# Kernel tuning notes

Hardware: AMD Instinct MI355X
Metric: run time of the kernel (lower is better)

Reference implementation:

```python
import jax, jax.numpy as jnp
import numpy as np

N_QUBITS = 4
N_LAYERS = 2


def setup_inputs() -> dict:
    key = jax.random.key(0)
    ks = jax.random.split(key, 8)
    B, S, D, H, O = 64, 4096, 20, 64, 3
    rn = lambda k, shape: jax.random.normal(k, shape, dtype=jnp.float32)
    sc = lambda fan: np.float32(1.0 / np.sqrt(fan))
    return {
        "x": rn(ks[0], (B, S, D)),
        "W_embed": rn(ks[1], (H, D)) * sc(D),
        "b_embed": jnp.zeros((H,), jnp.float32),
        "W_c2q": rn(ks[2], (N_QUBITS, H)) * sc(H),
        "b_c2q": jnp.zeros((N_QUBITS,), jnp.float32),
        "q_weights": rn(ks[3], (N_LAYERS, N_QUBITS, 3)) * np.float32(0.1),
        "W_q2c": rn(ks[4], (H, N_QUBITS)) * sc(N_QUBITS),
        "b_q2c": jnp.zeros((H,), jnp.float32),
        "W_out": rn(ks[5], (O, H)) * sc(H),
        "b_out": jnp.zeros((O,), jnp.float32),
    }


def _rot_matrix(phi, theta, omega):
    # PennyLane Rot(phi, theta, omega) = RZ(omega) @ RY(theta) @ RZ(phi)
    c = jnp.cos(theta * 0.5)
    s = jnp.sin(theta * 0.5)
    ep = jnp.exp(-0.5j * (phi + omega))  # e^{-i(phi+omega)/2}
    em = jnp.exp(-0.5j * (phi - omega))  # e^{-i(phi-omega)/2}
    row0 = jnp.stack([ep * c, -jnp.conj(em) * s])
    row1 = jnp.stack([em * s, jnp.conj(ep) * c])
    return jnp.stack([row0, row1]).astype(jnp.complex64)  # [2,2]


def _apply_1q(state, U, q):
    # state: [N,2,2,2,2], U: [2,2] shared across the batch
    ax = 1 + q
    s = jnp.moveaxis(state, ax, -1)
    s = jnp.einsum('...a,ba->...b', s, U)
    return jnp.moveaxis(s, -1, ax)


def _cnot(state, q):
    # control qubit q (axis 1+q), target qubit q+1 (axis 2+q)
    ac = 1 + q
    s0 = jnp.take(state, 0, axis=ac)
    # after removing control axis, the target axis index becomes ac
    s1 = jnp.flip(jnp.take(state, 1, axis=ac), axis=ac)
    return jnp.stack([s0, s1], axis=ac)


def _quantum_layer(q_in, weights):
    # q_in: [N, n_qubits] angles; weights: [n_layers, n_qubits, 3]
    half = q_in * 0.5
    v = jnp.stack([jnp.cos(half), jnp.sin(half)], axis=-1).astype(jnp.complex64)  # [N,4,2]
    # RY(inputs[i]) applied to |0...0> -> product state
    state = jnp.einsum('na,nb,nc,nd->nabcd', v[:, 0], v[:, 1], v[:, 2], v[:, 3])
    for layer in range(N_LAYERS):
        for q in range(N_QUBITS):
            U = _rot_matrix(weights[layer, q, 0], weights[layer, q, 1], weights[layer, q, 2])
            state = _apply_1q(state, U, q)
        for q in range(N_QUBITS - 1):
            state = _cnot(state, q)
    probs = state.real ** 2 + state.imag ** 2  # [N,2,2,2,2]
    z = []
    for q in range(N_QUBITS):
        axes = tuple(a for a in range(1, N_QUBITS + 1) if a != 1 + q)
        p = jnp.sum(probs, axis=axes)  # [N,2]
        z.append(p[:, 0] - p[:, 1])   # <Z_q>
    return jnp.stack(z, axis=-1)  # [N, n_qubits]


def reference(x, W_embed, b_embed, W_c2q, b_c2q, q_weights, W_q2c, b_q2c, W_out, b_out):
    B, S, _ = x.shape
    h = jax.nn.relu(jnp.einsum('bsd,hd->bsh', x, W_embed) + b_embed)      # [B,S,H]
    q_in = jnp.tanh(jnp.einsum('bsh,qh->bsq', h, W_c2q) + b_c2q)          # [B,S,4]
    z = _quantum_layer(q_in.reshape(B * S, N_QUBITS), q_weights)          # [B*S,4]
    z = z.reshape(B, S, N_QUBITS)
    h2 = jnp.einsum('bsq,hq->bsh', z, W_q2c) + b_q2c                      # [B,S,H]
    coords = jnp.einsum('bsh,oh->bso', h2, W_out) + b_out                 # [B,S,3]
    return coords
```

## Files before the change

### kernel.cpp

```cpp
#include <hip/hip_runtime.h>

typedef __bf16 bf16x8 __attribute__((ext_vector_type(8)));
typedef float f32x4 __attribute__((ext_vector_type(4)));
typedef float f32x2 __attribute__((ext_vector_type(2)));

__device__ __attribute__((aligned(16))) float g_C01[162];
__device__ float g_C2[81];
__device__ float g_off[3];

#define NQ 4
#define NLAYERS 2

__global__ __launch_bounds__(256) void precompute_kernel(
    const float* __restrict__ qw,
    const float* __restrict__ Wq2c,
    const float* __restrict__ bq2c,
    const float* __restrict__ Wout,
    const float* __restrict__ bout) {
  __shared__ float Ucoef[8][8];
  __shared__ float Ur[16][16];
  __shared__ float Ui[16][16];
  __shared__ float A[4][16][16];
  __shared__ float Wc[3][4];
  const int tid = threadIdx.x;

  if (tid < 64) {
    const int gate = tid >> 3, comp = tid & 7;
    const float phi   = qw[gate * 3 + 0];
    const float theta = qw[gate * 3 + 1];
    const float omega = qw[gate * 3 + 2];
    const float cs = (comp == 2 || comp == 3 || comp == 4 || comp == 5)
                         ? __sinf(0.5f * theta)
                         : __cosf(0.5f * theta);
    const float ang = (comp == 2 || comp == 3 || comp == 4 || comp == 5)
                          ? -0.5f * (phi - omega)
                          : -0.5f * (phi + omega);
    const float tr = ((comp & 1) == 0) ? __cosf(ang) : __sinf(ang);
    const float sgn = (comp == 2 || comp == 7) ? -1.f : 1.f;
    Ucoef[gate][comp] = sgn * tr * cs;
  }
  __syncthreads();

  const int col = tid >> 4, amp = tid & 15;
  float re = (amp == col) ? 1.f : 0.f, im = 0.f;
#pragma unroll
  for (int layer = 0; layer < NLAYERS; ++layer) {
#pragma unroll
    for (int q = 0; q < NQ; ++q) {
      const int gate = layer * NQ + q;
      const int bit = 8 >> q;
      const bool lo = !(amp & bit);
      const float cr1 = lo ? Ucoef[gate][0] : Ucoef[gate][6];
      const float ci1 = lo ? Ucoef[gate][1] : Ucoef[gate][7];
      const float cr2 = lo ? Ucoef[gate][2] : Ucoef[gate][4];
      const float ci2 = lo ? Ucoef[gate][3] : Ucoef[gate][5];
      const float pr = __shfl_xor(re, bit);
      const float pi = __shfl_xor(im, bit);
      const float mr = re, mi = im;
      re = cr1 * mr - ci1 * mi + cr2 * pr - ci2 * pi;
      im = cr1 * mi + ci1 * mr + cr2 * pi + ci2 * pr;
    }
#pragma unroll
    for (int q = 0; q < NQ - 1; ++q) {
      const int cb = 8 >> q, tb = 4 >> q;
      const float pr = __shfl_xor(re, tb);
      const float pi = __shfl_xor(im, tb);
      if (amp & cb) { re = pr; im = pi; }
    }
  }
  Ur[amp][col] = re;
  Ui[amp][col] = im;
  __syncthreads();

  for (int e = tid; e < 4 * 16 * 16; e += blockDim.x) {
    const int q = e >> 8, i = (e >> 4) & 15, j = e & 15;
    float s = 0.f;
    for (int k = 0; k < 16; ++k) {
      const float d = ((k >> (3 - q)) & 1) ? -1.f : 1.f;
      s += d * (Ur[k][i] * Ur[k][j] + Ui[k][i] * Ui[k][j]);
    }
    A[q][i][j] = s;
  }
  if (tid < 12) {
    const int o = tid >> 2, q = tid & 3;
    float s = 0.f;
    for (int h = 0; h < 64; ++h) s += Wout[o * 64 + h] * Wq2c[h * 4 + q];
    Wc[o][q] = s;
  }
  if (tid < 3) {
    float s = bout[tid];
    for (int h = 0; h < 64; ++h) s += Wout[tid * 64 + h] * bq2c[h];
    g_off[tid] = s;
  }
  __syncthreads();

  for (int e = tid; e < 243; e += blockDim.x) {
    const int o = e / 81, t = e % 81;
    const int tv0 = t / 27, tv1 = (t / 9) % 3, tv2 = (t / 3) % 3, tv3 = t % 3;
    const int tv[4] = {tv0, tv1, tv2, tv3};
    int xmask = 0, zmask = 0;
    for (int q = 0; q < 4; ++q) {
      const int b = 8 >> q;
      if (tv[q] == 2) xmask |= b;
      else if (tv[q] == 1) zmask |= b;
    }
    float s = 0.f;
    for (int i = 0; i < 16; ++i) {
      const int j = i ^ xmask;
      const float sgn = (__popc(i & zmask) & 1) ? -1.f : 1.f;
      const float g = Wc[o][0] * A[0][i][j] + Wc[o][1] * A[1][i][j] +
                      Wc[o][2] * A[2][i][j] + Wc[o][3] * A[3][i][j];
      s += sgn * g;
    }
    const float val = s * 0.0625f;
    if (o == 0) g_C01[2 * t] = val;
    else if (o == 1) g_C01[2 * t + 1] = val;
    else g_C2[t] = val;
  }
}

__device__ __forceinline__ float fast_tanh(float v) {
  const float e = __expf(2.f * v);
  return 1.f - 2.f * __builtin_amdgcn_rcpf(e + 1.f);
}

__global__ __launch_bounds__(256, 4) void fused_kernel(
    const float* __restrict__ x,
    const float* __restrict__ Wemb,
    const float* __restrict__ bemb,
    const float* __restrict__ Wc2q,
    const float* __restrict__ bc2q,
    float* __restrict__ out, int N) {
  __shared__ float xs[4][1280];

  const int tid = blockIdx.x * 256 + threadIdx.x;
  const int lane = threadIdx.x & 63;
  const int warp = threadIdx.x >> 6;
  const int wbase = (tid >> 6) << 6;
  if (wbase >= N) return;
  const int g = lane >> 4;
  const int cc = lane & 15;

  const f32x4 zero4 = {0.f, 0.f, 0.f, 0.f};

  {
    const float4* x4 = reinterpret_cast<const float4*>(x);
    float4* ls4 = reinterpret_cast<float4*>(&xs[warp][0]);
    const size_t base4 = (size_t)wbase * 5;
    const size_t max4 = (size_t)N * 5 - 1;
#pragma unroll
    for (int i = 0; i < 5; ++i) {
      size_t gi = base4 + (size_t)(i * 64 + lane);
      ls4[i * 64 + lane] = x4[gi <= max4 ? gi : max4];
    }
  }

  bf16x8 Aemb[4];
#pragma unroll
  for (int ht = 0; ht < 4; ++ht) {
    const int h = ht * 16 + cc;
    const float* wr = Wemb + h * 20;
    float t0 = 0.f, t1 = 0.f, t2 = 0.f, t3 = 0.f, t4 = 0.f, t5 = 0.f, t6 = 0.f, t7 = 0.f;
    if (g < 2) {
      const float4 v0 = *(const float4*)(wr + g * 8);
      const float4 v1 = *(const float4*)(wr + g * 8 + 4);
      t0 = v0.x; t1 = v0.y; t2 = v0.z; t3 = v0.w;
      t4 = v1.x; t5 = v1.y; t6 = v1.z; t7 = v1.w;
    } else if (g == 2) {
      const float4 v0 = *(const float4*)(wr + 16);
      t0 = v0.x; t1 = v0.y; t2 = v0.z; t3 = v0.w;
      t4 = bemb[h];
    }
    Aemb[ht][0] = (__bf16)t0; Aemb[ht][1] = (__bf16)t1;
    Aemb[ht][2] = (__bf16)t2; Aemb[ht][3] = (__bf16)t3;
    Aemb[ht][4] = (__bf16)t4; Aemb[ht][5] = (__bf16)t5;
    Aemb[ht][6] = (__bf16)t6; Aemb[ht][7] = (__bf16)t7;
  }

  bf16x8 A2[2];
#pragma unroll
  for (int t = 0; t < 2; ++t) {
#pragma unroll
    for (int j = 0; j < 8; ++j) {
      const int mu = t * 32 + ((j >> 2) << 4) + (g << 2) + (j & 3);
      A2[t][j] = (__bf16)Wc2q[(cc & 3) * 64 + mu];
    }
  }

  f32x4 av = zero4;
#pragma unroll
  for (int rt = 0; rt < 4; ++rt) {
    const int el = rt * 16 + cc;
    const float* ep = &xs[warp][el * 20];
    float t0 = 0.f, t1 = 0.f, t2 = 0.f, t3 = 0.f, t4 = 0.f, t5 = 0.f, t6 = 0.f, t7 = 0.f;
    if (g < 2) {
      const float4 v0 = *(const float4*)(ep + g * 8);
      const float4 v1 = *(const float4*)(ep + g * 8 + 4);
      t0 = v0.x; t1 = v0.y; t2 = v0.z; t3 = v0.w;
      t4 = v1.x; t5 = v1.y; t6 = v1.z; t7 = v1.w;
    } else if (g == 2) {
      const float4 v0 = *(const float4*)(ep + 16);
      t0 = v0.x; t1 = v0.y; t2 = v0.z; t3 = v0.w;
      t4 = 1.f;
    }
    bf16x8 B;
    B[0] = (__bf16)t0; B[1] = (__bf16)t1; B[2] = (__bf16)t2; B[3] = (__bf16)t3;
    B[4] = (__bf16)t4; B[5] = (__bf16)t5; B[6] = (__bf16)t6; B[7] = (__bf16)t7;

    const f32x4 acc0 = __builtin_amdgcn_mfma_f32_16x16x32_bf16(Aemb[0], B, zero4, 0, 0, 0);
    const f32x4 acc1 = __builtin_amdgcn_mfma_f32_16x16x32_bf16(Aemb[1], B, zero4, 0, 0, 0);
    const f32x4 acc2 = __builtin_amdgcn_mfma_f32_16x16x32_bf16(Aemb[2], B, zero4, 0, 0, 0);
    const f32x4 acc3 = __builtin_amdgcn_mfma_f32_16x16x32_bf16(Aemb[3], B, zero4, 0, 0, 0);

    bf16x8 P0, P1;
#pragma unroll
    for (int j = 0; j < 8; ++j) {
      P0[j] = (__bf16)fmaxf(((j >> 2) ? acc1 : acc0)[j & 3], 0.f);
      P1[j] = (__bf16)fmaxf(((j >> 2) ? acc3 : acc2)[j & 3], 0.f);
    }
    f32x4 a2 = __builtin_amdgcn_mfma_f32_16x16x32_bf16(A2[0], P0, zero4, 0, 0, 0);
    a2 = __builtin_amdgcn_mfma_f32_16x16x32_bf16(A2[1], P1, a2, 0, 0, 0);

    if (g == rt) av = a2;
  }

  const float a0 = fast_tanh(av[0] + bc2q[0]);
  const float a1 = fast_tanh(av[1] + bc2q[1]);
  const float a2v = fast_tanh(av[2] + bc2q[2]);
  const float a3 = fast_tanh(av[3] + bc2q[3]);

  const float f0v[3] = {1.f, __cosf(a0), __sinf(a0)};
  const float f1v[3] = {1.f, __cosf(a1), __sinf(a1)};
  const float f2v[3] = {1.f, __cosf(a2v), __sinf(a2v)};
  const float f3v[3] = {1.f, __cosf(a3), __sinf(a3)};

  float T23[9];
#pragma unroll
  for (int i2 = 0; i2 < 3; ++i2)
#pragma unroll
    for (int i3 = 0; i3 < 3; ++i3) T23[i2 * 3 + i3] = f2v[i2] * f3v[i3];
  float T[27];
#pragma unroll
  for (int i1 = 0; i1 < 3; ++i1)
#pragma unroll
    for (int k = 0; k < 9; ++k) T[i1 * 9 + k] = f1v[i1] * T23[k];

  f32x2 y01 = {g_off[0], g_off[1]};
  float y2 = g_off[2];
#pragma unroll
  for (int i0 = 0; i0 < 3; ++i0) {
    f32x2 s01 = {0.f, 0.f};
    float s2 = 0.f;
#pragma unroll
    for (int k = 0; k < 27; ++k) {
      const float tv = T[k];
      const f32x2 c01 = *reinterpret_cast<const f32x2*>(&g_C01[2 * (i0 * 27 + k)]);
      s01 += c01 * tv;
      s2 = fmaf(g_C2[i0 * 27 + k], tv, s2);
    }
    y01 += s01 * f0v[i0];
    y2 = fmaf(f0v[i0], s2, y2);
  }

  const int eo = wbase + lane;
  if (eo < N) {
    out[eo * 3 + 0] = y01[0];
    out[eo * 3 + 1] = y01[1];
    out[eo * 3 + 2] = y2;
  }
}

extern "C" void kernel_launch(void* const* d_in, const int* in_sizes, int n_in,
                              void* d_out, int out_size, void* d_ws, size_t ws_size,
                              hipStream_t stream) {
  const float* x    = (const float*)d_in[0];
  const float* Wemb = (const float*)d_in[1];
  const float* bemb = (const float*)d_in[2];
  const float* Wc2q = (const float*)d_in[3];
  const float* bc2q = (const float*)d_in[4];
  const float* qw   = (const float*)d_in[5];
  const float* Wq2c = (const float*)d_in[6];
  const float* bq2c = (const float*)d_in[7];
  const float* Wout = (const float*)d_in[8];
  const float* bout = (const float*)d_in[9];
  float* out = (float*)d_out;

  const int N = in_sizes[0] / 20;

  hipLaunchKernelGGL(precompute_kernel, dim3(1), dim3(256), 0, stream,
                     qw, Wq2c, bq2c, Wout, bout);
  hipLaunchKernelGGL(fused_kernel, dim3((N + 255) / 256), dim3(256), 0, stream,
                     x, Wemb, bemb, Wc2q, bc2q, out, N);
}
```

Measured before the change: 20.74 us.

## Fuse precompute into main kernel, stage x via registers with swizzled LDS, vectorize stores

Removes the separate single-block precompute launch and has every block recompute the quantum-circuit coefficient tables in shared memory, overlapping with its x loads. The sign-weighted A matrices are collapsed into three G matrices using per-output weights, reducing work per block. The x tile is loaded into registers first and written to LDS with an XOR swizzle and padding so the bias/zero lanes need no branches. Coefficients are read as float4 from LDS and outputs are staged through LDS for coalesced float4 stores. Redundant per-block precompute and extra syncthreads add cost in exchange for removing a kernel launch and serialization.

Result: slower. 25.42 us (+22.5%).

```diff
diff --git a/kernel.cpp b/kernel.cpp
--- a/kernel.cpp
+++ b/kernel.cpp
@@ -4,120 +4,15 @@
 typedef float f32x4 __attribute__((ext_vector_type(4)));
 typedef float f32x2 __attribute__((ext_vector_type(2)));
 
-__device__ __attribute__((aligned(16))) float g_C01[162];
-__device__ float g_C2[81];
-__device__ float g_off[3];
-
 #define NQ 4
 #define NLAYERS 2
 
-__global__ __launch_bounds__(256) void precompute_kernel(
-    const float* __restrict__ qw,
-    const float* __restrict__ Wq2c,
-    const float* __restrict__ bq2c,
-    const float* __restrict__ Wout,
-    const float* __restrict__ bout) {
-  __shared__ float Ucoef[8][8];
-  __shared__ float Ur[16][16];
-  __shared__ float Ui[16][16];
-  __shared__ float A[4][16][16];
-  __shared__ float Wc[3][4];
-  const int tid = threadIdx.x;
-
-  if (tid < 64) {
-    const int gate = tid >> 3, comp = tid & 7;
-    const float phi   = qw[gate * 3 + 0];
-    const float theta = qw[gate * 3 + 1];
-    const float omega = qw[gate * 3 + 2];
-    const float cs = (comp == 2 || comp == 3 || comp == 4 || comp == 5)
-                         ? __sinf(0.5f * theta)
-                         : __cosf(0.5f * theta);
-    const float ang = (comp == 2 || comp == 3 || comp == 4 || comp == 5)
-                          ? -0.5f * (phi - omega)
-                          : -0.5f * (phi + omega);
-    const float tr = ((comp & 1) == 0) ? __cosf(ang) : __sinf(ang);
-    const float sgn = (comp == 2 || comp == 7) ? -1.f : 1.f;
-    Ucoef[gate][comp] = sgn * tr * cs;
-  }
-  __syncthreads();
-
-  const int col = tid >> 4, amp = tid & 15;
-  float re = (amp == col) ? 1.f : 0.f, im = 0.f;
-#pragma unroll
-  for (int layer = 0; layer < NLAYERS; ++layer) {
-#pragma unroll
-    for (int q = 0; q < NQ; ++q) {
-      const int gate = layer * NQ + q;
-      const int bit = 8 >> q;
-      const bool lo = !(amp & bit);
-      const float cr1 = lo ? Ucoef[gate][0] : Ucoef[gate][6];
-      const float ci1 = lo ? Ucoef[gate][1] : Ucoef[gate][7];
-      const float cr2 = lo ? Ucoef[gate][2] : Ucoef[gate][4];
-      const float ci2 = lo ? Ucoef[gate][3] : Ucoef[gate][5];
-      const float pr = __shfl_xor(re, bit);
-      const float pi = __shfl_xor(im, bit);
-      const float mr = re, mi = im;
-      re = cr1 * mr - ci1 * mi + cr2 * pr - ci2 * pi;
-      im = cr1 * mi + ci1 * mr + cr2 * pi + ci2 * pr;
-    }
-#pragma unroll
-    for (int q = 0; q < NQ - 1; ++q) {
-      const int cb = 8 >> q, tb = 4 >> q;
-      const float pr = __shfl_xor(re, tb);
-      const float pi = __shfl_xor(im, tb);
-      if (amp & cb) { re = pr; im = pi; }
-    }
-  }
-  Ur[amp][col] = re;
-  Ui[amp][col] = im;
-  __syncthreads();
-
-  for (int e = tid; e < 4 * 16 * 16; e += blockDim.x) {
-    const int q = e >> 8, i = (e >> 4) & 15, j = e & 15;
-    float s = 0.f;
-    for (int k = 0; k < 16; ++k) {
-      const float d = ((k >> (3 - q)) & 1) ? -1.f : 1.f;
-      s += d * (Ur[k][i] * Ur[k][j] + Ui[k][i] * Ui[k][j]);
-    }
-    A[q][i][j] = s;
-  }
-  if (tid < 12) {
-    const int o = tid >> 2, q = tid & 3;
-    float s = 0.f;
-    for (int h = 0; h < 64; ++h) s += Wout[o * 64 + h] * Wq2c[h * 4 + q];
-    Wc[o][q] = s;
-  }
-  if (tid < 3) {
-    float s = bout[tid];
-    for (int h = 0; h < 64; ++h) s += Wout[tid * 64 + h] * bq2c[h];
-    g_off[tid] = s;
-  }
-  __syncthreads();
-
-  for (int e = tid; e < 243; e += blockDim.x) {
-    const int o = e / 81, t = e % 81;
-    const int tv0 = t / 27, tv1 = (t / 9) % 3, tv2 = (t / 3) % 3, tv3 = t % 3;
-    const int tv[4] = {tv0, tv1, tv2, tv3};
-    int xmask = 0, zmask = 0;
-    for (int q = 0; q < 4; ++q) {
-      const int b = 8 >> q;
-      if (tv[q] == 2) xmask |= b;
-      else if (tv[q] == 1) zmask |= b;
-    }
-    float s = 0.f;
-    for (int i = 0; i < 16; ++i) {
-      const int j = i ^ xmask;
-      const float sgn = (__popc(i & zmask) & 1) ? -1.f : 1.f;
-      const float g = Wc[o][0] * A[0][i][j] + Wc[o][1] * A[1][i][j] +
-                      Wc[o][2] * A[2][i][j] + Wc[o][3] * A[3][i][j];
-      s += sgn * g;
-    }
-    const float val = s * 0.0625f;
-    if (o == 0) g_C01[2 * t] = val;
-    else if (o == 1) g_C01[2 * t + 1] = val;
-    else g_C2[t] = val;
-  }
-}
+#define OFF_UCOEF 0
+#define OFF_WC    64
+#define OFF_UR    96
+#define OFF_UI    352
+#define OFF_W     608
+#define OFF_G     704
 
 __device__ __forceinline__ float fast_tanh(float v) {
   const float e = __expf(2.f * v);
@@ -130,28 +25,37 @@
     const float* __restrict__ bemb,
     const float* __restrict__ Wc2q,
     const float* __restrict__ bc2q,
+    const float* __restrict__ qw,
+    const float* __restrict__ Wq2c,
+    const float* __restrict__ bq2c,
+    const float* __restrict__ Wout,
+    const float* __restrict__ bout,
     float* __restrict__ out, int N) {
-  __shared__ float xs[4][1280];
-
-  const int tid = blockIdx.x * 256 + threadIdx.x;
-  const int lane = threadIdx.x & 63;
-  const int warp = threadIdx.x >> 6;
-  const int wbase = (tid >> 6) << 6;
-  if (wbase >= N) return;
+  __shared__ __attribute__((aligned(16))) float smem[4 * 2048];
+  __shared__ __attribute__((aligned(16))) float Cs01[3 * 56];
+  __shared__ __attribute__((aligned(16))) float Cs2[3 * 28];
+  __shared__ float offsS[3];
+
+  if ((int)(blockIdx.x << 8) >= N) return;
+
+  const int tid = threadIdx.x;
+  const int lane = tid & 63;
+  const int warp = tid >> 6;
+  const int wbase = (int)(blockIdx.x << 8) + (warp << 6);
   const int g = lane >> 4;
   const int cc = lane & 15;
-
+  float* ws = &smem[warp * 2048];
   const f32x4 zero4 = {0.f, 0.f, 0.f, 0.f};
 
+  float4 xr[5];
   {
     const float4* x4 = reinterpret_cast<const float4*>(x);
-    float4* ls4 = reinterpret_cast<float4*>(&xs[warp][0]);
+    const size_t max4 = (size_t)N * 5 - 1;
     const size_t base4 = (size_t)wbase * 5;
-    const size_t max4 = (size_t)N * 5 - 1;
 #pragma unroll
     for (int i = 0; i < 5; ++i) {
       size_t gi = base4 + (size_t)(i * 64 + lane);
-      ls4[i * 64 + lane] = x4[gi <= max4 ? gi : max4];
+      xr[i] = x4[gi <= max4 ? gi : max4];
     }
   }
 
@@ -187,25 +91,143 @@
     }
   }
 
+  if (tid < 64) {
+    const int gate = tid >> 3, comp = tid & 7;
+    const float phi   = qw[gate * 3 + 0];
+    const float theta = qw[gate * 3 + 1];
+    const float omega = qw[gate * 3 + 2];
+    const bool mid = (comp >= 2 && comp <= 5);
+    const float cs = mid ? __sinf(0.5f * theta) : __cosf(0.5f * theta);
+    const float ang = mid ? -0.5f * (phi - omega) : -0.5f * (phi + omega);
+    const float tr = ((comp & 1) == 0) ? __cosf(ang) : __sinf(ang);
+    const float sgn = (comp == 2 || comp == 7) ? -1.f : 1.f;
+    smem[OFF_UCOEF + gate * 8 + comp] = sgn * tr * cs;
+  } else if (tid < 76) {
+    const int e = tid - 64, o = e >> 2, q = e & 3;
+    float s = 0.f;
+    for (int h = 0; h < 64; ++h) s += Wout[o * 64 + h] * Wq2c[h * 4 + q];
+    smem[OFF_WC + e] = s;
+  } else if (tid < 79) {
+    const int o = tid - 76;
+    float s = bout[o];
+    for (int h = 0; h < 64; ++h) s += Wout[o * 64 + h] * bq2c[h];
+    offsS[o] = s;
+  }
+  __syncthreads();
+
+  {
+    const int col = tid >> 4, amp = tid & 15;
+    float re = (amp == col) ? 1.f : 0.f, im = 0.f;
+#pragma unroll
+    for (int layer = 0; layer < NLAYERS; ++layer) {
+#pragma unroll
+      for (int q = 0; q < NQ; ++q) {
+        const int gate = layer * NQ + q;
+        const int bit = 8 >> q;
+        const bool lo = !(amp & bit);
+        const float cr1 = smem[OFF_UCOEF + gate * 8 + (lo ? 0 : 6)];
+        const float ci1 = smem[OFF_UCOEF + gate * 8 + (lo ? 1 : 7)];
+        const float cr2 = smem[OFF_UCOEF + gate * 8 + (lo ? 2 : 4)];
+        const float ci2 = smem[OFF_UCOEF + gate * 8 + (lo ? 3 : 5)];
+        const float pr = __shfl_xor(re, bit);
+        const float pi = __shfl_xor(im, bit);
+        const float mr = re, mi = im;
+        re = cr1 * mr - ci1 * mi + cr2 * pr - ci2 * pi;
+        im = cr1 * mi + ci1 * mr + cr2 * pi + ci2 * pr;
+      }
+#pragma unroll
+      for (int q = 0; q < NQ - 1; ++q) {
+        const int cb = 8 >> q, tb = 4 >> q;
+        const float pr = __shfl_xor(re, tb);
+        const float pi = __shfl_xor(im, tb);
+        if (amp & cb) { re = pr; im = pi; }
+      }
+    }
+    smem[OFF_UR + amp * 16 + col] = re;
+    smem[OFF_UI + amp * 16 + col] = im;
+  }
+  if (tid < 48) {
+    const int o = tid >> 4, k = tid & 15;
+    float s = 0.f;
+#pragma unroll
+    for (int q = 0; q < NQ; ++q) {
+      const float t = smem[OFF_WC + o * 4 + q];
+      s += ((k >> (3 - q)) & 1) ? -t : t;
+    }
+    smem[OFF_W + tid] = s;
+  }
+  __syncthreads();
+
+  {
+    const int i = tid >> 4, j = tid & 15;
+    float s0 = 0.f, s1 = 0.f, s2 = 0.f;
+#pragma unroll
+    for (int k = 0; k < 16; ++k) {
+      const float S = smem[OFF_UR + k * 16 + i] * smem[OFF_UR + k * 16 + j] +
+                      smem[OFF_UI + k * 16 + i] * smem[OFF_UI + k * 16 + j];
+      s0 = fmaf(smem[OFF_W + k], S, s0);
+      s1 = fmaf(smem[OFF_W + 16 + k], S, s1);
+      s2 = fmaf(smem[OFF_W + 32 + k], S, s2);
+    }
+    smem[OFF_G + (i * 16 + j)] = s0;
+    smem[OFF_G + 256 + (i * 16 + j)] = s1;
+    smem[OFF_G + 512 + (i * 16 + j)] = s2;
+  }
+  __syncthreads();
+
+  if (tid < 243) {
+    const int o = tid / 81, t = tid % 81;
+    const int tv0 = t / 27, tv1 = (t / 9) % 3, tv2 = (t / 3) % 3, tv3 = t % 3;
+    const int tv[4] = {tv0, tv1, tv2, tv3};
+    int xmask = 0, zmask = 0;
+#pragma unroll
+    for (int q = 0; q < 4; ++q) {
+      const int b = 8 >> q;
+      if (tv[q] == 2) xmask |= b;
+      else if (tv[q] == 1) zmask |= b;
+    }
+    float s = 0.f;
+#pragma unroll
+    for (int i = 0; i < 16; ++i) {
+      const float sgn = (__popc(i & zmask) & 1) ? -1.f : 1.f;
+      s += sgn * smem[OFF_G + o * 256 + i * 16 + (i ^ xmask)];
+    }
+    const float val = s * 0.0625f;
+    if (o < 2) Cs01[tv0 * 56 + 2 * (t % 27) + o] = val;
+    else Cs2[tv0 * 28 + (t % 27)] = val;
+  } else if (tid < 249) {
+    const int p = tid - 243;
+    Cs01[(p >> 1) * 56 + 54 + (p & 1)] = 0.f;
+  } else if (tid < 252) {
+    Cs2[(tid - 249) * 28 + 27] = 0.f;
+  }
+  __syncthreads();
+
+  {
+#pragma unroll
+    for (int i = 0; i < 5; ++i) {
+      const int m = i * 64 + lane;
+      const int el = m / 5, ch = m % 5;
+      *(float4*)&ws[el * 32 + ((ch * 4) ^ ((el & 7) << 2))] = xr[i];
+    }
+    const float4 bias4 = {1.f, 0.f, 0.f, 0.f};
+    const float4 z4 = {0.f, 0.f, 0.f, 0.f};
+    const int sw = (lane & 7) << 2;
+    *(float4*)&ws[lane * 32 + ((5 * 4) ^ sw)] = bias4;
+    *(float4*)&ws[lane * 32 + ((6 * 4) ^ sw)] = z4;
+    *(float4*)&ws[lane * 32 + ((7 * 4) ^ sw)] = z4;
+  }
+
   f32x4 av = zero4;
 #pragma unroll
   for (int rt = 0; rt < 4; ++rt) {
     const int el = rt * 16 + cc;
-    const float* ep = &xs[warp][el * 20];
-    float t0 = 0.f, t1 = 0.f, t2 = 0.f, t3 = 0.f, t4 = 0.f, t5 = 0.f, t6 = 0.f, t7 = 0.f;
-    if (g < 2) {
-      const float4 v0 = *(const float4*)(ep + g * 8);
-      const float4 v1 = *(const float4*)(ep + g * 8 + 4);
-      t0 = v0.x; t1 = v0.y; t2 = v0.z; t3 = v0.w;
-      t4 = v1.x; t5 = v1.y; t6 = v1.z; t7 = v1.w;
-    } else if (g == 2) {
-      const float4 v0 = *(const float4*)(ep + 16);
-      t0 = v0.x; t1 = v0.y; t2 = v0.z; t3 = v0.w;
-      t4 = 1.f;
-    }
+    const int sw = (el & 7) << 2;
+    const float4 u0 = *(const float4*)&ws[el * 32 + ((g * 8 + 0) ^ sw)];
+    const float4 u1 = *(const float4*)&ws[el * 32 + ((g * 8 + 4) ^ sw)];
     bf16x8 B;
-    B[0] = (__bf16)t0; B[1] = (__bf16)t1; B[2] = (__bf16)t2; B[3] = (__bf16)t3;
-    B[4] = (__bf16)t4; B[5] = (__bf16)t5; B[6] = (__bf16)t6; B[7] = (__bf16)t7;
+    B[0] = (__bf16)u0.x; B[1] = (__bf16)u0.y; B[2] = (__bf16)u0.z; B[3] = (__bf16)u0.w;
+    B[4] = (__bf16)u1.x; B[5] = (__bf16)u1.y; B[6] = (__bf16)u1.z; B[7] = (__bf16)u1.w;
 
     const f32x4 acc0 = __builtin_amdgcn_mfma_f32_16x16x32_bf16(Aemb[0], B, zero4, 0, 0, 0);
     const f32x4 acc1 = __builtin_amdgcn_mfma_f32_16x16x32_bf16(Aemb[1], B, zero4, 0, 0, 0);
@@ -239,34 +261,54 @@
   for (int i2 = 0; i2 < 3; ++i2)
 #pragma unroll
     for (int i3 = 0; i3 < 3; ++i3) T23[i2 * 3 + i3] = f2v[i2] * f3v[i3];
-  float T[27];
+  float T[28];
 #pragma unroll
   for (int i1 = 0; i1 < 3; ++i1)
 #pragma unroll
     for (int k = 0; k < 9; ++k) T[i1 * 9 + k] = f1v[i1] * T23[k];
-
-  f32x2 y01 = {g_off[0], g_off[1]};
-  float y2 = g_off[2];
+  T[27] = 0.f;
+
+  f32x2 y01 = {offsS[0], offsS[1]};
+  float y2 = offsS[2];
 #pragma unroll
   for (int i0 = 0; i0 < 3; ++i0) {
     f32x2 s01 = {0.f, 0.f};
-    float s2 = 0.f;
-#pragma unroll
-    for (int k = 0; k < 27; ++k) {
-      const float tv = T[k];
-      const f32x2 c01 = *reinterpret_cast<const f32x2*>(&g_C01[2 * (i0 * 27 + k)]);
-      s01 += c01 * tv;
-      s2 = fmaf(g_C2[i0 * 27 + k], tv, s2);
+#pragma unroll
+    for (int kk = 0; kk < 14; ++kk) {
+      const float4 cp = *(const float4*)&Cs01[i0 * 56 + kk * 4];
+      const f32x2 lo = {cp.x, cp.y};
+      const f32x2 hi = {cp.z, cp.w};
+      s01 += lo * T[2 * kk];
+      s01 += hi * T[2 * kk + 1];
+    }
+    float s2v = 0.f;
+#pragma unroll
+    for (int kk = 0; kk < 7; ++kk) {
+      const float4 c2 = *(const float4*)&Cs2[i0 * 28 + kk * 4];
+      s2v = fmaf(c2.x, T[4 * kk + 0], s2v);
+      s2v = fmaf(c2.y, T[4 * kk + 1], s2v);
+      s2v = fmaf(c2.z, T[4 * kk + 2], s2v);
+      s2v = fmaf(c2.w, T[4 * kk + 3], s2v);
     }
     y01 += s01 * f0v[i0];
-    y2 = fmaf(f0v[i0], s2, y2);
-  }
-
-  const int eo = wbase + lane;
-  if (eo < N) {
-    out[eo * 3 + 0] = y01[0];
-    out[eo * 3 + 1] = y01[1];
-    out[eo * 3 + 2] = y2;
+    y2 = fmaf(f0v[i0], s2v, y2);
+  }
+
+  if (wbase + 64 <= N) {
+    ws[lane * 3 + 0] = y01[0];
+    ws[lane * 3 + 1] = y01[1];
+    ws[lane * 3 + 2] = y2;
+    if (lane < 48) {
+      const float4 v = *(const float4*)&ws[lane * 4];
+      reinterpret_cast<float4*>(out + (size_t)wbase * 3)[lane] = v;
+    }
+  } else {
+    const int eo = wbase + lane;
+    if (eo < N) {
+      out[eo * 3 + 0] = y01[0];
+      out[eo * 3 + 1] = y01[1];
+      out[eo * 3 + 2] = y2;
+    }
   }
 }
 
@@ -287,8 +329,6 @@
 
   const int N = in_sizes[0] / 20;
 
-  hipLaunchKernelGGL(precompute_kernel, dim3(1), dim3(256), 0, stream,
-                     qw, Wq2c, bq2c, Wout, bout);
   hipLaunchKernelGGL(fused_kernel, dim3((N + 255) / 256), dim3(256), 0, stream,
-                     x, Wemb, bemb, Wc2q, bc2q, out, N);
+                     x, Wemb, bemb, Wc2q, bc2q, qw, Wq2c, bq2c, Wout, bout, out, N);
 }
```

## Load x directly into LDS, fold biases into MFMA accumulators, coalesce output stores

Applied to the files above, without the earlier changes.

Full warps now move x tiles with global_load_lds straight into shared memory, skipping the register round trip. The embedding and c2q biases go into the MFMA accumulator inputs instead of an extra K element and scalar adds. Outputs are staged in LDS and written as coalesced float4 stores. The risks are the explicit vmcnt wait, which stalls until all loads finish, and extra bias loads inside the loop.

Measured after the change: 25.70 us. +23.9%, slower.

```diff
diff --git a/kernel.cpp b/kernel.cpp
--- a/kernel.cpp
+++ b/kernel.cpp
@@ -131,7 +131,7 @@
     const float* __restrict__ Wc2q,
     const float* __restrict__ bc2q,
     float* __restrict__ out, int N) {
-  __shared__ float xs[4][1280];
+  __shared__ __attribute__((aligned(16))) float smem[4][1280];
 
   const int tid = blockIdx.x * 256 + threadIdx.x;
   const int lane = threadIdx.x & 63;
@@ -140,18 +140,27 @@
   if (wbase >= N) return;
   const int g = lane >> 4;
   const int cc = lane & 15;
+  float* ws = &smem[warp][0];
+  const bool full = (wbase + 64 <= N);
 
   const f32x4 zero4 = {0.f, 0.f, 0.f, 0.f};
 
-  {
-    const float4* x4 = reinterpret_cast<const float4*>(x);
-    float4* ls4 = reinterpret_cast<float4*>(&xs[warp][0]);
-    const size_t base4 = (size_t)wbase * 5;
-    const size_t max4 = (size_t)N * 5 - 1;
+  if (full) {
+    const float4* x4 = reinterpret_cast<const float4*>(x) + (size_t)wbase * 5;
 #pragma unroll
     for (int i = 0; i < 5; ++i) {
-      size_t gi = base4 + (size_t)(i * 64 + lane);
-      ls4[i * 64 + lane] = x4[gi <= max4 ? gi : max4];
+      __builtin_amdgcn_global_load_lds(
+          (const __attribute__((address_space(1))) void*)(x4 + i * 64 + lane),
+          (__attribute__((address_space(3))) void*)(ws + i * 256), 16, 0, 0);
+    }
+  } else {
+#pragma unroll
+    for (int i = 0; i < 5; ++i) {
+      const int m = i * 64 + lane;
+      const int eg = wbase + m / 5;
+      float4 v = make_float4(0.f, 0.f, 0.f, 0.f);
+      if (eg < N) v = reinterpret_cast<const float4*>(x)[(size_t)eg * 5 + m % 5];
+      *(float4*)&ws[m * 4] = v;
     }
   }
 
@@ -169,7 +178,6 @@
     } else if (g == 2) {
       const float4 v0 = *(const float4*)(wr + 16);
       t0 = v0.x; t1 = v0.y; t2 = v0.z; t3 = v0.w;
-      t4 = bemb[h];
     }
     Aemb[ht][0] = (__bf16)t0; Aemb[ht][1] = (__bf16)t1;
     Aemb[ht][2] = (__bf16)t2; Aemb[ht][3] = (__bf16)t3;
@@ -187,47 +195,53 @@
     }
   }
 
+  const float4 bq = *(const float4*)bc2q;
+  f32x4 Cq;
+  Cq[0] = bq.x; Cq[1] = bq.y; Cq[2] = bq.z; Cq[3] = bq.w;
+
+  asm volatile("s_waitcnt vmcnt(0)" ::: "memory");
+
   f32x4 av = zero4;
 #pragma unroll
   for (int rt = 0; rt < 4; ++rt) {
     const int el = rt * 16 + cc;
-    const float* ep = &xs[warp][el * 20];
-    float t0 = 0.f, t1 = 0.f, t2 = 0.f, t3 = 0.f, t4 = 0.f, t5 = 0.f, t6 = 0.f, t7 = 0.f;
+    bf16x8 B;
+#pragma unroll
+    for (int j = 0; j < 8; ++j) B[j] = (__bf16)0.f;
     if (g < 2) {
-      const float4 v0 = *(const float4*)(ep + g * 8);
-      const float4 v1 = *(const float4*)(ep + g * 8 + 4);
-      t0 = v0.x; t1 = v0.y; t2 = v0.z; t3 = v0.w;
-      t4 = v1.x; t5 = v1.y; t6 = v1.z; t7 = v1.w;
+      const float4 u0 = *(const float4*)&ws[el * 20 + g * 8];
+      const float4 u1 = *(const float4*)&ws[el * 20 + g * 8 + 4];
+      B[0] = (__bf16)u0.x; B[1] = (__bf16)u0.y; B[2] = (__bf16)u0.z; B[3] = (__bf16)u0.w;
+      B[4] = (__bf16)u1.x; B[5] = (__bf16)u1.y; B[6] = (__bf16)u1.z; B[7] = (__bf16)u1.w;
     } else if (g == 2) {
-      const float4 v0 = *(const float4*)(ep + 16);
-      t0 = v0.x; t1 = v0.y; t2 = v0.z; t3 = v0.w;
-      t4 = 1.f;
-    }
-    bf16x8 B;
-    B[0] = (__bf16)t0; B[1] = (__bf16)t1; B[2] = (__bf16)t2; B[3] = (__bf16)t3;
-    B[4] = (__bf16)t4; B[5] = (__bf16)t5; B[6] = (__bf16)t6; B[7] = (__bf16)t7;
-
-    const f32x4 acc0 = __builtin_amdgcn_mfma_f32_16x16x32_bf16(Aemb[0], B, zero4, 0, 0, 0);
-    const f32x4 acc1 = __builtin_amdgcn_mfma_f32_16x16x32_bf16(Aemb[1], B, zero4, 0, 0, 0);
-    const f32x4 acc2 = __builtin_amdgcn_mfma_f32_16x16x32_bf16(Aemb[2], B, zero4, 0, 0, 0);
-    const f32x4 acc3 = __builtin_amdgcn_mfma_f32_16x16x32_bf16(Aemb[3], B, zero4, 0, 0, 0);
+      const float4 u0 = *(const float4*)&ws[el * 20 + 16];
+      B[0] = (__bf16)u0.x; B[1] = (__bf16)u0.y; B[2] = (__bf16)u0.z; B[3] = (__bf16)u0.w;
+    }
+
+    f32x4 acc[4];
+#pragma unroll
+    for (int ht = 0; ht < 4; ++ht) {
+      const float4 bi = *(const float4*)(bemb + ht * 16 + g * 4);
+      f32x4 ci; ci[0] = bi.x; ci[1] = bi.y; ci[2] = bi.z; ci[3] = bi.w;
+      acc[ht] = __builtin_amdgcn_mfma_f32_16x16x32_bf16(Aemb[ht], B, ci, 0, 0, 0);
+    }
 
     bf16x8 P0, P1;
 #pragma unroll
     for (int j = 0; j < 8; ++j) {
-      P0[j] = (__bf16)fmaxf(((j >> 2) ? acc1 : acc0)[j & 3], 0.f);
-      P1[j] = (__bf16)fmaxf(((j >> 2) ? acc3 : acc2)[j & 3], 0.f);
-    }
-    f32x4 a2 = __builtin_amdgcn_mfma_f32_16x16x32_bf16(A2[0], P0, zero4, 0, 0, 0);
+      P0[j] = (__bf16)fmaxf(((j >> 2) ? acc[1] : acc[0])[j & 3], 0.f);
+      P1[j] = (__bf16)fmaxf(((j >> 2) ? acc[3] : acc[2])[j & 3], 0.f);
+    }
+    f32x4 a2 = __builtin_amdgcn_mfma_f32_16x16x32_bf16(A2[0], P0, Cq, 0, 0, 0);
     a2 = __builtin_amdgcn_mfma_f32_16x16x32_bf16(A2[1], P1, a2, 0, 0, 0);
 
     if (g == rt) av = a2;
   }
 
-  const float a0 = fast_tanh(av[0] + bc2q[0]);
-  const float a1 = fast_tanh(av[1] + bc2q[1]);
-  const float a2v = fast_tanh(av[2] + bc2q[2]);
-  const float a3 = fast_tanh(av[3] + bc2q[3]);
+  const float a0 = fast_tanh(av[0]);
+  const float a1 = fast_tanh(av[1]);
+  const float a2v = fast_tanh(av[2]);
+  const float a3 = fast_tanh(av[3]);
 
   const float f0v[3] = {1.f, __cosf(a0), __sinf(a0)};
   const float f1v[3] = {1.f, __cosf(a1), __sinf(a1)};
@@ -262,11 +276,21 @@
     y2 = fmaf(f0v[i0], s2, y2);
   }
 
-  const int eo = wbase + lane;
-  if (eo < N) {
-    out[eo * 3 + 0] = y01[0];
-    out[eo * 3 + 1] = y01[1];
-    out[eo * 3 + 2] = y2;
+  if (full) {
+    ws[lane * 3 + 0] = y01[0];
+    ws[lane * 3 + 1] = y01[1];
+    ws[lane * 3 + 2] = y2;
+    if (lane < 48) {
+      const float4 v = *(const float4*)&ws[lane * 4];
+      reinterpret_cast<float4*>(out + (size_t)wbase * 3)[lane] = v;
+    }
+  } else {
+    const int eo = wbase + lane;
+    if (eo < N) {
+      out[eo * 3 + 0] = y01[0];
+      out[eo * 3 + 1] = y01[1];
+      out[eo * 3 + 2] = y2;
+    }
   }
 }
 
```

## Process two 64-row groups per warp with prefetched x and swizzled LDS layout

Applied to the files above, without the earlier changes.

Each warp now handles two groups of 64 rows. The second group's x tile is loaded into registers while the first group's MFMA pipeline runs, so global load latency is hidden and the per-warp weight-fragment setup is amortized over twice as many rows. The LDS staging layout changes to a 32-float padded, XOR-swizzled row with the bias/zero padding written explicitly, which removes the g-dependent branches when building B fragments. The grid is halved, and the extra registers and larger shared tile may reduce occupancy.

After: 26.83 us. 29.3% more time.

```diff
diff --git a/kernel.cpp b/kernel.cpp
--- a/kernel.cpp
+++ b/kernel.cpp
@@ -124,6 +124,116 @@
   return 1.f - 2.f * __builtin_amdgcn_rcpf(e + 1.f);
 }
 
+
+__device__ __forceinline__ void load_x_group(const float* __restrict__ x,
+                                             int wbase, int lane, int N,
+                                             float4 xr[5]) {
+  const float4* x4 = reinterpret_cast<const float4*>(x);
+  const size_t max4 = (size_t)N * 5 - 1;
+  const size_t base4 = (size_t)wbase * 5;
+#pragma unroll
+  for (int i = 0; i < 5; ++i) {
+    size_t gi = base4 + (size_t)(i * 64 + lane);
+    xr[i] = x4[gi <= max4 ? gi : max4];
+  }
+}
+
+__device__ __forceinline__ void stage_x(float* ws, int lane, const float4 xr[5]) {
+#pragma unroll
+  for (int i = 0; i < 5; ++i) {
+    const int m = i * 64 + lane;
+    const int el = m / 5, ch = m % 5;
+    *(float4*)&ws[el * 32 + ((ch * 4) ^ ((el & 7) << 2))] = xr[i];
+  }
+  const float4 bias4 = {1.f, 0.f, 0.f, 0.f};
+  const float4 z4 = {0.f, 0.f, 0.f, 0.f};
+  const int sw = (lane & 7) << 2;
+  *(float4*)&ws[lane * 32 + ((5 * 4) ^ sw)] = bias4;
+  *(float4*)&ws[lane * 32 + ((6 * 4) ^ sw)] = z4;
+  *(float4*)&ws[lane * 32 + ((7 * 4) ^ sw)] = z4;
+}
+
+__device__ __forceinline__ f32x4 compute_group(const float* ws, int g, int cc,
+                                               const bf16x8 Aemb[4],
+                                               const bf16x8 A2[2]) {
+  const f32x4 zero4 = {0.f, 0.f, 0.f, 0.f};
+  f32x4 av = zero4;
+#pragma unroll
+  for (int rt = 0; rt < 4; ++rt) {
+    const int el = rt * 16 + cc;
+    const int sw = (el & 7) << 2;
+    const float4 u0 = *(const float4*)&ws[el * 32 + ((g * 8 + 0) ^ sw)];
+    const float4 u1 = *(const float4*)&ws[el * 32 + ((g * 8 + 4) ^ sw)];
+    bf16x8 B;
+    B[0] = (__bf16)u0.x; B[1] = (__bf16)u0.y; B[2] = (__bf16)u0.z; B[3] = (__bf16)u0.w;
+    B[4] = (__bf16)u1.x; B[5] = (__bf16)u1.y; B[6] = (__bf16)u1.z; B[7] = (__bf16)u1.w;
+
+    const f32x4 acc0 = __builtin_amdgcn_mfma_f32_16x16x32_bf16(Aemb[0], B, zero4, 0, 0, 0);
+    const f32x4 acc1 = __builtin_amdgcn_mfma_f32_16x16x32_bf16(Aemb[1], B, zero4, 0, 0, 0);
+    const f32x4 acc2 = __builtin_amdgcn_mfma_f32_16x16x32_bf16(Aemb[2], B, zero4, 0, 0, 0);
+    const f32x4 acc3 = __builtin_amdgcn_mfma_f32_16x16x32_bf16(Aemb[3], B, zero4, 0, 0, 0);
+
+    bf16x8 P0, P1;
+#pragma unroll
+    for (int j = 0; j < 8; ++j) {
+      P0[j] = (__bf16)fmaxf(((j >> 2) ? acc1 : acc0)[j & 3], 0.f);
+      P1[j] = (__bf16)fmaxf(((j >> 2) ? acc3 : acc2)[j & 3], 0.f);
+    }
+    f32x4 a2 = __builtin_amdgcn_mfma_f32_16x16x32_bf16(A2[0], P0, zero4, 0, 0, 0);
+    a2 = __builtin_amdgcn_mfma_f32_16x16x32_bf16(A2[1], P1, a2, 0, 0, 0);
+
+    if (g == rt) av = a2;
+  }
+  return av;
+}
+
+__device__ __forceinline__ void tail_store(f32x4 av, const float* __restrict__ bc2q,
+                                           float* __restrict__ out, int eo, int N) {
+  const float a0 = fast_tanh(av[0] + bc2q[0]);
+  const float a1 = fast_tanh(av[1] + bc2q[1]);
+  const float a2v = fast_tanh(av[2] + bc2q[2]);
+  const float a3 = fast_tanh(av[3] + bc2q[3]);
+
+  const float f0v[3] = {1.f, __cosf(a0), __sinf(a0)};
+  const float f1v[3] = {1.f, __cosf(a1), __sinf(a1)};
+  const float f2v[3] = {1.f, __cosf(a2v), __sinf(a2v)};
+  const float f3v[3] = {1.f, __cosf(a3), __sinf(a3)};
+
+  float T23[9];
+#pragma unroll
+  for (int i2 = 0; i2 < 3; ++i2)
+#pragma unroll
+    for (int i3 = 0; i3 < 3; ++i3) T23[i2 * 3 + i3] = f2v[i2] * f3v[i3];
+  float T[27];
+#pragma unroll
+  for (int i1 = 0; i1 < 3; ++i1)
+#pragma unroll
+    for (int k = 0; k < 9; ++k) T[i1 * 9 + k] = f1v[i1] * T23[k];
+
+  f32x2 y01 = {g_off[0], g_off[1]};
+  float y2 = g_off[2];
+#pragma unroll
+  for (int i0 = 0; i0 < 3; ++i0) {
+    f32x2 s01 = {0.f, 0.f};
+    float s2 = 0.f;
+#pragma unroll
+    for (int k = 0; k < 27; ++k) {
+      const float tv = T[k];
+      const f32x2 c01 = *reinterpret_cast<const f32x2*>(&g_C01[2 * (i0 * 27 + k)]);
+      s01 += c01 * tv;
+      s2 = fmaf(g_C2[i0 * 27 + k], tv, s2);
+    }
+    y01 += s01 * f0v[i0];
+    y2 = fmaf(f0v[i0], s2, y2);
+  }
+
+  if (eo < N) {
+    out[eo * 3 + 0] = y01[0];
+    out[eo * 3 + 1] = y01[1];
+    out[eo * 3 + 2] = y2;
+  }
+}
+
 __global__ __launch_bounds__(256, 4) void fused_kernel(
     const float* __restrict__ x,
     const float* __restrict__ Wemb,
@@ -131,29 +241,19 @@
     const float* __restrict__ Wc2q,
     const float* __restrict__ bc2q,
     float* __restrict__ out, int N) {
-  __shared__ float xs[4][1280];
-
-  const int tid = blockIdx.x * 256 + threadIdx.x;
+  __shared__ __attribute__((aligned(16))) float smem[4][2048];
+
   const int lane = threadIdx.x & 63;
   const int warp = threadIdx.x >> 6;
-  const int wbase = (tid >> 6) << 6;
-  if (wbase >= N) return;
+  const int wbase0 = (int)((blockIdx.x * 4 + warp) << 7);
+  if (wbase0 >= N) return;
+  const int wbase1 = wbase0 + 64;
   const int g = lane >> 4;
   const int cc = lane & 15;
-
-  const f32x4 zero4 = {0.f, 0.f, 0.f, 0.f};
-
-  {
-    const float4* x4 = reinterpret_cast<const float4*>(x);
-    float4* ls4 = reinterpret_cast<float4*>(&xs[warp][0]);
-    const size_t base4 = (size_t)wbase * 5;
-    const size_t max4 = (size_t)N * 5 - 1;
-#pragma unroll
-    for (int i = 0; i < 5; ++i) {
-      size_t gi = base4 + (size_t)(i * 64 + lane);
-      ls4[i * 64 + lane] = x4[gi <= max4 ? gi : max4];
-    }
-  }
+  float* ws = &smem[warp][0];
+
+  float4 xr0[5];
+  load_x_group(x, wbase0, lane, N, xr0);
 
   bf16x8 Aemb[4];
 #pragma unroll
@@ -187,86 +287,21 @@
     }
   }
 
-  f32x4 av = zero4;
-#pragma unroll
-  for (int rt = 0; rt < 4; ++rt) {
-    const int el = rt * 16 + cc;
-    const float* ep = &xs[warp][el * 20];
-    float t0 = 0.f, t1 = 0.f, t2 = 0.f, t3 = 0.f, t4 = 0.f, t5 = 0.f, t6 = 0.f, t7 = 0.f;
-    if (g < 2) {
-      const float4 v0 = *(const float4*)(ep + g * 8);
-      const float4 v1 = *(const float4*)(ep + g * 8 + 4);
-      t0 = v0.x; t1 = v0.y; t2 = v0.z; t3 = v0.w;
-      t4 = v1.x; t5 = v1.y; t6 = v1.z; t7 = v1.w;
-    } else if (g == 2) {
-      const float4 v0 = *(const float4*)(ep + 16);
-      t0 = v0.x; t1 = v0.y; t2 = v0.z; t3 = v0.w;
-      t4 = 1.f;
-    }
-    bf16x8 B;
-    B[0] = (__bf16)t0; B[1] = (__bf16)t1; B[2] = (__bf16)t2; B[3] = (__bf16)t3;
-    B[4] = (__bf16)t4; B[5] = (__bf16)t5; B[6] = (__bf16)t6; B[7] = (__bf16)t7;
-
-    const f32x4 acc0 = __builtin_amdgcn_mfma_f32_16x16x32_bf16(Aemb[0], B, zero4, 0, 0, 0);
-    const f32x4 acc1 = __builtin_amdgcn_mfma_f32_16x16x32_bf16(Aemb[1], B, zero4, 0, 0, 0);
-    const f32x4 acc2 = __builtin_amdgcn_mfma_f32_16x16x32_bf16(Aemb[2], B, zero4, 0, 0, 0);
-    const f32x4 acc3 = __builtin_amdgcn_mfma_f32_16x16x32_bf16(Aemb[3], B, zero4, 0, 0, 0);
-
-    bf16x8 P0, P1;
-#pragma unroll
-    for (int j = 0; j < 8; ++j) {
-      P0[j] = (__bf16)fmaxf(((j >> 2) ? acc1 : acc0)[j & 3], 0.f);
-      P1[j] = (__bf16)fmaxf(((j >> 2) ? acc3 : acc2)[j & 3], 0.f);
-    }
-    f32x4 a2 = __builtin_amdgcn_mfma_f32_16x16x32_bf16(A2[0], P0, zero4, 0, 0, 0);
-    a2 = __builtin_amdgcn_mfma_f32_16x16x32_bf16(A2[1], P1, a2, 0, 0, 0);
-
-    if (g == rt) av = a2;
-  }
-
-  const float a0 = fast_tanh(av[0] + bc2q[0]);
-  const float a1 = fast_tanh(av[1] + bc2q[1]);
-  const float a2v = fast_tanh(av[2] + bc2q[2]);
-  const float a3 = fast_tanh(av[3] + bc2q[3]);
-
-  const float f0v[3] = {1.f, __cosf(a0), __sinf(a0)};
-  const float f1v[3] = {1.f, __cosf(a1), __sinf(a1)};
-  const float f2v[3] = {1.f, __cosf(a2v), __sinf(a2v)};
-  const float f3v[3] = {1.f, __cosf(a3), __sinf(a3)};
-
-  float T23[9];
-#pragma unroll
-  for (int i2 = 0; i2 < 3; ++i2)
-#pragma unroll
-    for (int i3 = 0; i3 < 3; ++i3) T23[i2 * 3 + i3] = f2v[i2] * f3v[i3];
-  float T[27];
-#pragma unroll
-  for (int i1 = 0; i1 < 3; ++i1)
-#pragma unroll
-    for (int k = 0; k < 9; ++k) T[i1 * 9 + k] = f1v[i1] * T23[k];
-
-  f32x2 y01 = {g_off[0], g_off[1]};
-  float y2 = g_off[2];
-#pragma unroll
-  for (int i0 = 0; i0 < 3; ++i0) {
-    f32x2 s01 = {0.f, 0.f};
-    float s2 = 0.f;
-#pragma unroll
-    for (int k = 0; k < 27; ++k) {
-      const float tv = T[k];
-      const f32x2 c01 = *reinterpret_cast<const f32x2*>(&g_C01[2 * (i0 * 27 + k)]);
-      s01 += c01 * tv;
-      s2 = fmaf(g_C2[i0 * 27 + k], tv, s2);
-    }
-    y01 += s01 * f0v[i0];
-    y2 = fmaf(f0v[i0], s2, y2);
-  }
-
-  const int eo = wbase + lane;
-  if (eo < N) {
-    out[eo * 3 + 0] = y01[0];
-    out[eo * 3 + 1] = y01[1];
-    out[eo * 3 + 2] = y2;
+  stage_x(ws, lane, xr0);
+
+  float4 xr1[5];
+  const bool has1 = (wbase1 < N);
+  if (has1) load_x_group(x, wbase1, lane, N, xr1);
+
+  const f32x4 av0 = compute_group(ws, g, cc, Aemb, A2);
+
+  if (has1) {
+    stage_x(ws, lane, xr1);
+    tail_store(av0, bc2q, out, wbase0 + lane, N);
+    const f32x4 av1 = compute_group(ws, g, cc, Aemb, A2);
+    tail_store(av1, bc2q, out, wbase1 + lane, N);
+  } else {
+    tail_store(av0, bc2q, out, wbase0 + lane, N);
   }
 }
 
@@ -289,6 +324,6 @@
 
   hipLaunchKernelGGL(precompute_kernel, dim3(1), dim3(256), 0, stream,
                      qw, Wq2c, bq2c, Wout, bout);
-  hipLaunchKernelGGL(fused_kernel, dim3((N + 255) / 256), dim3(256), 0, stream,
+  hipLaunchKernelGGL(fused_kernel, dim3((N + 511) / 512), dim3(256), 0, stream,
                      x, Wemb, bemb, Wc2q, bc2q, out, N);
 }
```
